# Performance work log

Measured on AMD Instinct MI355X. Metric: run time of the kernel, lower is better.

Reference implementation:

```python
import jax, jax.numpy as jnp
import numpy as np

E, H, T_MAX = 1024, 16, 2048
HS = E // H
EPS = 1e-5


def _layernorm(x, g, b):
    m = jnp.mean(x, axis=-1, keepdims=True)
    v = jnp.mean(jnp.square(x - m), axis=-1, keepdims=True)
    return (x - m) * jax.lax.rsqrt(v + EPS) * g + b


def setup_inputs() -> dict:
    key = jax.random.key(0)
    ks = jax.random.split(key, 8)
    B, T = 2, 2048
    s = 0.02
    return {
        "x": jax.random.normal(ks[0], (B, T, E), jnp.float32),
        "ln1_g": jnp.ones((E,), jnp.float32),
        "ln1_b": jnp.zeros((E,), jnp.float32),
        "Wk": jax.random.normal(ks[1], (H, E, HS), jnp.float32) * s,  # stacked per-head key weights (x @ Wk)
        "Wv": jax.random.normal(ks[2], (H, E, HS), jnp.float32) * s,
        "Wproj": jax.random.normal(ks[3], (E, E), jnp.float32) * s,
        "bproj": jnp.zeros((E,), jnp.float32),
        "ln2_g": jnp.ones((E,), jnp.float32),
        "ln2_b": jnp.zeros((E,), jnp.float32),
        "W1": jax.random.normal(ks[4], (E, 4 * E), jnp.float32) * s,
        "b1": jnp.zeros((4 * E,), jnp.float32),
        "W2": jax.random.normal(ks[5], (4 * E, E), jnp.float32) * s,
        "b2": jnp.zeros((E,), jnp.float32),
    }


def reference(x, ln1_g, ln1_b, Wk, Wv, Wproj, bproj, ln2_g, ln2_b, W1, b1, W2, b2):
    B, T, C = x.shape
    h = _layernorm(x, ln1_g, ln1_b)
    # NOTE: original code uses the KEY projection for both q and k (q = self.key(x))
    k = jnp.einsum('bte,hed->bhtd', h, Wk)
    q = k
    wei = jnp.einsum('bhtd,bhsd->bhts', q, k) * (C ** -0.5)  # scale by full n_embd, as in source
    causal = jnp.tril(jnp.ones((T, T), bool))
    wei = jnp.where(causal, wei, -jnp.inf)
    # source applies softmax over dim=1 (the query/row axis of the TxT matrix)
    wei = jax.nn.softmax(wei, axis=2)
    v = jnp.einsum('bte,hed->bhtd', h, Wv)
    attn = jnp.einsum('bhts,bhsd->bhtd', wei, v)          # [B,H,T,HS]
    attn = attn.transpose(0, 2, 1, 3).reshape(B, T, C)    # concat heads
    x = x + attn @ Wproj + bproj
    h2 = _layernorm(x, ln2_g, ln2_b)
    x = x + jax.nn.relu(h2 @ W1 + b1) @ W2 + b2
    return x
```

## Files before the change

kernel.cpp:

```cpp
#include <hip/hip_runtime.h>

using bf16x8 = __attribute__((ext_vector_type(8))) __bf16;
using f32x4  = __attribute__((ext_vector_type(4))) float;

__device__ __forceinline__ f32x4 mfma16(bf16x8 a, bf16x8 b, f32x4 c) {
  return __builtin_amdgcn_mfma_f32_16x16x32_bf16(a, b, c, 0, 0, 0);
}

__device__ __forceinline__ unsigned short f2bf(float f) {
  union { float f; unsigned int u; } x; x.f = f;
  unsigned int u = x.u + 0x7FFFu + ((x.u >> 16) & 1u);
  return (unsigned short)(u >> 16);
}

__device__ __forceinline__ unsigned int cvtpk_bf16(float lo, float hi) {
  unsigned int r;
  asm("v_cvt_pk_bf16_f32 %0, %1, %2" : "=v"(r) : "v"(lo), "v"(hi));
  return r;
}

__device__ __forceinline__ float fexp2(float x) {
#if __has_builtin(__builtin_amdgcn_exp2f)
  return __builtin_amdgcn_exp2f(x);
#else
  float r; asm("v_exp_f32 %0, %1" : "=v"(r) : "v"(x)); return r;
#endif
}

__device__ __forceinline__ void gl_lds16(const unsigned short* g, unsigned short* l) {
  __builtin_amdgcn_global_load_lds(
      (__attribute__((address_space(1))) void*)(g),
      (__attribute__((address_space(3))) void*)(l), 16, 0, 0);
}

__device__ __forceinline__ bf16x8 rdsw64(const unsigned short* base, int r, int ch) {
  int c = ch ^ (r & 7);
  return *reinterpret_cast<const bf16x8*>(base + ((size_t)r * 8 + c) * 8);
}

__global__ __launch_bounds__(256) void transpose_cvt(const float* __restrict__ in,
                                                     unsigned short* __restrict__ out,
                                                     int R, int C) {
  __shared__ float t[32][33];
  int b = blockIdx.z;
  const float* inb = in + (size_t)b * R * C;
  unsigned short* outb = out + (size_t)b * R * C;
  int tx = threadIdx.x & 31, ty = threadIdx.x >> 5;
  int c0 = blockIdx.x * 32, r0 = blockIdx.y * 32;
#pragma unroll
  for (int i = 0; i < 4; ++i)
    t[ty + i * 8][tx] = inb[(size_t)(r0 + ty + i * 8) * C + c0 + tx];
  __syncthreads();
#pragma unroll
  for (int i = 0; i < 4; ++i)
    outb[(size_t)(c0 + ty + i * 8) * R + r0 + tx] = f2bf(t[tx][ty + i * 8]);
}

__global__ __launch_bounds__(256) void ln_bf16(const float* __restrict__ x,
                                               const float* __restrict__ g,
                                               const float* __restrict__ bta,
                                               unsigned short* __restrict__ out) {
  int row = blockIdx.x, tid = threadIdx.x;
  float4 v = reinterpret_cast<const float4*>(x + (size_t)row * 1024)[tid];
  float s = v.x + v.y + v.z + v.w;
  float s2 = v.x * v.x + v.y * v.y + v.z * v.z + v.w * v.w;
#pragma unroll
  for (int m = 1; m < 64; m <<= 1) { s += __shfl_xor(s, m); s2 += __shfl_xor(s2, m); }
  __shared__ float red[8];
  int w = tid >> 6;
  if ((tid & 63) == 0) { red[w] = s; red[w + 4] = s2; }
  __syncthreads();
  s  = red[0] + red[1] + red[2] + red[3];
  s2 = red[4] + red[5] + red[6] + red[7];
  float mean = s * (1.f / 1024.f);
  float var  = s2 * (1.f / 1024.f) - mean * mean;
  float rstd = rsqrtf(var + 1e-5f);
  float4 gv = reinterpret_cast<const float4*>(g)[tid];
  float4 bv = reinterpret_cast<const float4*>(bta)[tid];
  ushort4 o;
  o.x = f2bf((v.x - mean) * rstd * gv.x + bv.x);
  o.y = f2bf((v.y - mean) * rstd * gv.y + bv.y);
  o.z = f2bf((v.z - mean) * rstd * gv.z + bv.z);
  o.w = f2bf((v.w - mean) * rstd * gv.w + bv.w);
  reinterpret_cast<ushort4*>(out + (size_t)row * 1024)[tid] = o;
}

__device__ __forceinline__ void stage_half(const unsigned short* gbase, int K,
                                           unsigned short* lds, int tid) {
#pragma unroll
  for (int j = 0; j < 2; ++j) {
    int lr = j * 64 + (tid >> 3);
    int c  = (tid & 7) ^ (lr & 7);
    gl_lds16(gbase + (size_t)lr * K + c * 8, lds + (size_t)(j * 512 + tid) * 8);
  }
}

__device__ __forceinline__ bf16x8 rdfrag(const unsigned short* base, int r, int k) {
  return *reinterpret_cast<const bf16x8*>(base + ((size_t)r * 8 + (k ^ (r & 7))) * 8);
}

__global__ __launch_bounds__(512, 2) void gemm256_relu(const unsigned short* __restrict__ A,
                                                       const unsigned short* __restrict__ Bt,
                                                       unsigned short* __restrict__ C,
                                                       const float* __restrict__ bias,
                                                       int M, int N, int K) {
  __shared__ __align__(16) unsigned short LA[2][256 * 64];
  __shared__ __align__(16) unsigned short LB[2][256 * 64];
  int tid = threadIdx.x, lane = tid & 63, w = tid >> 6;
  int l15 = lane & 15, lh = lane >> 4;
  int wr = (w >> 2) * 128, wc = (w & 3) * 64;
  int bid = blockIdx.x;
  int xcd = bid & 7, g = bid >> 3;
  int bm = (xcd >> 1) * 4 + (g >> 3);
  int bn = (xcd & 1) * 8 + (g & 7);
  const unsigned short* Ab = A + (size_t)(bm * 256) * K;
  const unsigned short* Bb = Bt + (size_t)(bn * 256) * K;
  f32x4 acc[8][4] = {};
  int NT = K >> 6;
  stage_half(Ab, K, &LA[0][0], tid);
  stage_half(Ab + (size_t)128 * K, K, &LA[0][128 * 64], tid);
  stage_half(Bb, K, &LB[0][0], tid);
  stage_half(Bb + (size_t)128 * K, K, &LB[0][128 * 64], tid);
  asm volatile("s_waitcnt vmcnt(0)" ::: "memory");
  __builtin_amdgcn_s_barrier();
  for (int t = 0; t < NT; ++t) {
    int cur = t & 1;
    const unsigned short* la = &LA[cur][0];
    const unsigned short* lb = &LB[cur][0];
    unsigned short* na = &LA[cur ^ 1][0];
    unsigned short* nb = &LB[cur ^ 1][0];
    int k0n = (t + 1) << 6;
    bool more = (t + 1 < NT);
    bf16x8 bfr[4][2];
#pragma unroll
    for (int q = 0; q < 4; ++q) {
      if (more) {
        if (q == 0)      stage_half(Ab + k0n, K, na, tid);
        else if (q == 1) stage_half(Ab + (size_t)128 * K + k0n, K, na + 128 * 64, tid);
        else if (q == 2) stage_half(Bb + k0n, K, nb, tid);
        else             stage_half(Bb + (size_t)128 * K + k0n, K, nb + 128 * 64, tid);
      }
      if (q == 0) {
        if (more) asm volatile("s_waitcnt vmcnt(2)" ::: "memory");
        else      asm volatile("s_waitcnt vmcnt(0)" ::: "memory");
        __builtin_amdgcn_s_barrier();
      }
      bf16x8 aq[2][2];
#pragma unroll
      for (int i = 0; i < 2; ++i)
#pragma unroll
        for (int kk = 0; kk < 2; ++kk)
          aq[i][kk] = rdfrag(la, wr + q * 32 + i * 16 + l15, kk * 4 + lh);
      if (q == 0) {
#pragma unroll
        for (int ni = 0; ni < 4; ++ni)
#pragma unroll
          for (int kk = 0; kk < 2; ++kk)
            bfr[ni][kk] = rdfrag(lb, wc + ni * 16 + l15, kk * 4 + lh);
      }
      if (q != 0) __builtin_amdgcn_s_barrier();
      __builtin_amdgcn_s_setprio(1);
#pragma unroll
      for (int kk = 0; kk < 2; ++kk)
#pragma unroll
        for (int i = 0; i < 2; ++i)
#pragma unroll
          for (int ni = 0; ni < 4; ++ni)
            acc[q * 2 + i][ni] = mfma16(aq[i][kk], bfr[ni][kk], acc[q * 2 + i][ni]);
      __builtin_amdgcn_s_setprio(0);
      __builtin_amdgcn_s_barrier();
    }
  }
#pragma unroll
  for (int mi = 0; mi < 8; ++mi)
#pragma unroll
    for (int ni = 0; ni < 4; ++ni) {
      int row0 = bm * 256 + wr + mi * 16 + lh * 4;
      int col  = bn * 256 + wc + ni * 16 + l15;
      float bv = bias[col];
#pragma unroll
      for (int r = 0; r < 4; ++r) {
        float v = fmaxf(acc[mi][ni][r] + bv, 0.f);
        C[(size_t)(row0 + r) * N + col] = f2bf(v);
      }
    }
}

#define GBK 128
#define KSCL 0.04508422f

__device__ __forceinline__ bf16x8 rd128(const unsigned short* base, int r, int ch) {
  int c = ch ^ ((r & 7) << 1);
  return *reinterpret_cast<const bf16x8*>(base + (size_t)r * GBK + c * 8);
}

template<int TM, int MODE>
__global__ __launch_bounds__(256) void gemm_bf16(const unsigned short* __restrict__ A,
                                                 const unsigned short* __restrict__ Bt,
                                                 void* __restrict__ Cout,
                                                 unsigned short* __restrict__ Cout2,
                                                 const float* __restrict__ bias,
                                                 const float* __restrict__ resid,
                                                 const float* __restrict__ scvec,
                                                 int M, int N, int K) {
  constexpr int MI = TM / 32;
  constexpr int AJ = TM / 16;
  __shared__ __align__(16) unsigned short Sh[(TM + 128) * GBK];
  unsigned short* As = Sh;
  unsigned short* Bs = Sh + TM * GBK;
  int tid = threadIdx.x;
  int lane = tid & 63, w = tid >> 6;
  int l15 = lane & 15, lh = lane >> 4;
  int wr = (w >> 1) * (TM / 2), wc = (w & 1) * 64;
  int nblk = N >> 7;
  int rows = M / TM;
  int bm, bn;
  if (nblk == 8 && (rows & 7) == 0) {
    int bid = blockIdx.x;
    int xcd = bid & 7, g = bid >> 3;
    bm = xcd * (rows >> 3) + (g >> 3);
    bn = g & 7;
  } else {
    bm = blockIdx.x / nblk; bn = blockIdx.x % nblk;
  }
  const unsigned short* ApJ[AJ];
  const unsigned short* BpJ[8];
#pragma unroll
  for (int j = 0; j < AJ; ++j) {
    int row = j * 16 + (tid >> 4);
    int ch  = (tid & 15) ^ ((row & 7) << 1);
    ApJ[j] = A + (size_t)(bm * TM + row) * K + ch * 8;
  }
#pragma unroll
  for (int j = 0; j < 8; ++j) {
    int row = j * 16 + (tid >> 4);
    int ch  = (tid & 15) ^ ((row & 7) << 1);
    BpJ[j] = Bt + (size_t)(bn * 128 + row) * K + ch * 8;
  }
  f32x4 acc[MI][4] = {};
  for (int k0 = 0; k0 < K; k0 += GBK) {
#pragma unroll
    for (int j = 0; j < AJ; ++j)
      gl_lds16(ApJ[j] + k0, &As[(j * 256 + tid) * 8]);
#pragma unroll
    for (int j = 0; j < 8; ++j)
      gl_lds16(BpJ[j] + k0, &Bs[(j * 256 + tid) * 8]);
    __syncthreads();
    bf16x8 af[MI][4], bfr[4][4];
#pragma unroll
    for (int i = 0; i < MI; ++i)
#pragma unroll
      for (int kk = 0; kk < 4; ++kk)
        af[i][kk] = rd128(As, wr + i * 16 + l15, kk * 4 + lh);
#pragma unroll
    for (int i = 0; i < 4; ++i)
#pragma unroll
      for (int kk = 0; kk < 4; ++kk)
        bfr[i][kk] = rd128(Bs, wc + i * 16 + l15, kk * 4 + lh);
#pragma unroll
    for (int kk = 0; kk < 4; ++kk)
#pragma unroll
      for (int mi = 0; mi < MI; ++mi)
#pragma unroll
        for (int ni = 0; ni < 4; ++ni)
          acc[mi][ni] = mfma16(af[mi][kk], bfr[ni][kk], acc[mi][ni]);
    __syncthreads();
  }
  if constexpr (MODE == 3) {
#pragma unroll
    for (int mi = 0; mi < MI; ++mi) {
#pragma unroll
      for (int ni = 0; ni < 4; ++ni) {
        int tl = wr + mi * 16 + lh * 4;
        int dl = wc + ni * 16 + l15;
        int colg = bn * 128 + dl;
        int bb = bm >> 5, hh = colg >> 6;
        const float* sp = scvec + (size_t)(bb * 16 + hh) * 2048 + (bm & 31) * 64 + tl;
        float4 rs = *reinterpret_cast<const float4*>(sp);
        unsigned int p0 = f2bf(acc[mi][ni][0] * rs.x) | ((unsigned int)f2bf(acc[mi][ni][1] * rs.y) << 16);
        unsigned int p1 = f2bf(acc[mi][ni][2] * rs.z) | ((unsigned int)f2bf(acc[mi][ni][3] * rs.w) << 16);
        uint2 pk = {p0, p1};
        *reinterpret_cast<uint2*>(&Sh[dl * 64 + (tl ^ ((dl & 7) << 3))]) = pk;
      }
    }
    __syncthreads();
    int dr = tid >> 1, th = (tid & 1) * 32;
    int bb = bm >> 5, tbase = (bm & 31) * 64;
    size_t colg = bn * 128 + dr;
    unsigned short* Vt = (unsigned short*)Cout;
#pragma unroll
    for (int j = 0; j < 4; ++j) {
      int t = th + j * 8;
      int4 v = *reinterpret_cast<const int4*>(&Sh[dr * 64 + (t ^ ((dr & 7) << 3))]);
      *reinterpret_cast<int4*>(&Vt[((size_t)bb * 1024 + colg) * 2048 + tbase + t]) = v;
    }
  } else {
#pragma unroll
    for (int mi = 0; mi < MI; ++mi) {
#pragma unroll
      for (int ni = 0; ni < 4; ++ni) {
        int row0 = bm * TM + wr + mi * 16 + lh * 4;
        int col  = bn * 128 + wc + ni * 16 + l15;
        float bv = (MODE == 2) ? 0.f : bias[col];
#pragma unroll
        for (int r = 0; r < 4; ++r) {
          int row = row0 + r;
          float v = acc[mi][ni][r] + bv;
          if constexpr (MODE == 0) {
            v += resid[(size_t)row * N + col];
            ((float*)Cout)[(size_t)row * N + col] = v;
          } else {
            ((unsigned short*)Cout)[(size_t)row * N + col] = f2bf(v);
            Cout2[(size_t)row * N + col] = f2bf(v * KSCL);
          }
        }
      }
    }
  }
}

__global__ __launch_bounds__(512) void attn_stats(const unsigned short* __restrict__ Kb,
                                                  const unsigned short* __restrict__ Kbs,
                                                  float* __restrict__ colrcp) {
  __shared__ __align__(16) unsigned short Kt[2][64 * 64];
  int bid = blockIdx.x;
  int q = bid >> 8, x = (bid >> 5) & 7, bh = bid & 31;
  int b = bh >> 4, h = bh & 15;
  int sb = q ? (15 - x) : x;
  int tid = threadIdx.x, lane = tid & 63, w = tid >> 6;
  int l15 = lane & 15, lh = lane >> 4;
  int s0 = sb * 128, sw = s0 + w * 16;
  const unsigned short* Kp  = Kb  + ((size_t)b * 2048) * 1024 + h * 64;
  const unsigned short* Kps = Kbs + ((size_t)b * 2048) * 1024 + h * 64;
  bf16x8 as[2];
#pragma unroll
  for (int kc = 0; kc < 2; ++kc)
    as[kc] = *reinterpret_cast<const bf16x8*>(Kp + (size_t)(sw + l15) * 1024 + kc * 32 + (lh << 3));
  int srow = tid >> 3;
  int sch  = (tid & 7) ^ (srow & 7);
  const unsigned short* ksrc = Kps + (size_t)srow * 1024 + sch * 8;
  gl_lds16(ksrc + (size_t)s0 * 1024, &Kt[0][tid * 8]);
  __syncthreads();
  float l[4] = {0.f, 0.f, 0.f, 0.f};
  int nt = 32 - 2 * sb;
  for (int it = 0; it < nt; ++it) {
    int t0 = s0 + it * 64;
    int cur = it & 1;
    if (it + 1 < nt)
      gl_lds16(ksrc + (size_t)(t0 + 64) * 1024, &Kt[cur ^ 1][tid * 8]);
    if (t0 + 63 >= sw) {
      bool dmask = (t0 < sw + 16);
#pragma unroll
      for (int tf = 0; tf < 4; ++tf) {
        int tr = tf * 16 + l15;
        bf16x8 bt0 = rdsw64(&Kt[cur][0], tr, lh);
        bf16x8 bt1 = rdsw64(&Kt[cur][0], tr, 4 + lh);
        f32x4 z = {};
        f32x4 sa = mfma16(as[1], bt1, mfma16(as[0], bt0, z));
        int tg = t0 + tr;
#pragma unroll
        for (int r = 0; r < 4; ++r) {
          float e = fexp2(sa[r]);
          if (dmask) { int sg = sw + lh * 4 + r; e = (tg >= sg) ? e : 0.f; }
          l[r] += e;
        }
      }
    }
    __syncthreads();
  }
#pragma unroll
  for (int m = 1; m < 16; m <<= 1)
#pragma unroll
    for (int r = 0; r < 4; ++r)
      l[r] += __shfl_xor(l[r], m);
  if (l15 == 0) {
#pragma unroll
    for (int r = 0; r < 4; ++r)
      colrcp[(size_t)bh * 2048 + sw + lh * 4 + r] = 1.f / l[r];
  }
}

__global__ __launch_bounds__(512) void attn_pv(const unsigned short* __restrict__ Kb,
                                               const unsigned short* __restrict__ Kbs,
                                               const unsigned short* __restrict__ Vt,
                                               unsigned short* __restrict__ attn) {
  __shared__ __align__(16) unsigned short Ks[2][64 * 64];
  __shared__ __align__(16) unsigned short Vs[2][64 * 64];
  __shared__ __align__(16) unsigned short Pl[8][16][68];
  int bid = blockIdx.x;
  int q = bid >> 8, x = (bid >> 5) & 7, bh = bid & 31;
  int b = bh >> 4, h = bh & 15;
  int tb = q ? (15 - x) : x;
  int tid = threadIdx.x, lane = tid & 63, w = tid >> 6;
  int l15 = lane & 15, lh = lane >> 4;
  int t0 = tb * 128, tw = t0 + w * 16;
  const unsigned short* Kp  = Kb  + ((size_t)b * 2048) * 1024 + h * 64;
  const unsigned short* Kps = Kbs + ((size_t)b * 2048) * 1024 + h * 64;
  const unsigned short* Vp  = Vt + (size_t)bh * 64 * 2048;
  bf16x8 at[2];
#pragma unroll
  for (int kc = 0; kc < 2; ++kc)
    at[kc] = *reinterpret_cast<const bf16x8*>(Kp + (size_t)(tw + l15) * 1024 + kc * 32 + (lh << 3));
  int srow = tid >> 3;
  int sch  = (tid & 7) ^ (srow & 7);
  const unsigned short* ksrc = Kps + (size_t)srow * 1024 + sch * 8;
  const unsigned short* vsrc = Vp + (size_t)srow * 2048 + sch * 8;
  gl_lds16(ksrc, &Ks[0][tid * 8]);
  gl_lds16(vsrc, &Vs[0][tid * 8]);
  __syncthreads();
  f32x4 acc[4] = {};
  int nt = 2 * tb + 2;
  for (int it = 0; it < nt; ++it) {
    int s0 = it * 64;
    int cur = it & 1;
    if (it + 1 < nt) {
      gl_lds16(ksrc + (size_t)(s0 + 64) * 1024, &Ks[cur ^ 1][tid * 8]);
      gl_lds16(vsrc + (s0 + 64), &Vs[cur ^ 1][tid * 8]);
    }
    if (s0 <= tw + 15) {
      bool dmask = (s0 + 63 > tw);
#pragma unroll
      for (int sf = 0; sf < 4; ++sf) {
        int sr = sf * 16 + l15;
        bf16x8 ks0 = rdsw64(&Ks[cur][0], sr, lh);
        bf16x8 ks1 = rdsw64(&Ks[cur][0], sr, 4 + lh);
        f32x4 z = {};
        f32x4 sa = mfma16(ks1, at[1], mfma16(ks0, at[0], z));
        float pe[4];
#pragma unroll
        for (int r = 0; r < 4; ++r) {
          float p = fexp2(sa[r]);
          if (dmask) {
            int sg = s0 + sf * 16 + lh * 4 + r;
            int tg = tw + l15;
            p = (sg <= tg) ? p : 0.f;
          }
          pe[r] = p;
        }
        unsigned int u0 = cvtpk_bf16(pe[0], pe[1]);
        unsigned int u1 = cvtpk_bf16(pe[2], pe[3]);
        unsigned long long pk = (unsigned long long)u0 | ((unsigned long long)u1 << 32);
        *reinterpret_cast<unsigned long long*>(&Pl[w][l15][sf * 16 + lh * 4]) = pk;
      }
#pragma unroll
      for (int c2 = 0; c2 < 2; ++c2) {
        bf16x8 pa = *reinterpret_cast<const bf16x8*>(&Pl[w][l15][c2 * 32 + (lh << 3)]);
#pragma unroll
        for (int nf = 0; nf < 4; ++nf) {
          int dr = nf * 16 + l15;
          bf16x8 vb = rdsw64(&Vs[cur][0], dr, c2 * 4 + lh);
          acc[nf] = mfma16(pa, vb, acc[nf]);
        }
      }
    }
    __syncthreads();
  }
#pragma unroll
  for (int nf = 0; nf < 4; ++nf)
#pragma unroll
    for (int r = 0; r < 4; ++r) {
      int t = tw + lh * 4 + r;
      attn[(size_t)(b * 2048 + t) * 1024 + h * 64 + nf * 16 + l15] = f2bf(acc[nf][r]);
    }
}

extern "C" void kernel_launch(void* const* d_in, const int* in_sizes, int n_in,
                              void* d_out, int out_size, void* d_ws, size_t ws_size,
                              hipStream_t stream) {
  (void)in_sizes; (void)n_in; (void)out_size; (void)ws_size;
  const float* x     = (const float*)d_in[0];
  const float* ln1_g = (const float*)d_in[1];
  const float* ln1_b = (const float*)d_in[2];
  const float* Wk    = (const float*)d_in[3];
  const float* Wv    = (const float*)d_in[4];
  const float* Wproj = (const float*)d_in[5];
  const float* bproj = (const float*)d_in[6];
  const float* ln2_g = (const float*)d_in[7];
  const float* ln2_b = (const float*)d_in[8];
  const float* W1    = (const float*)d_in[9];
  const float* b1    = (const float*)d_in[10];
  const float* W2    = (const float*)d_in[11];
  const float* b2    = (const float*)d_in[12];
  float* out = (float*)d_out;

  char* ws = (char*)d_ws;
  size_t off = 0;
  auto alloc = [&](size_t bytes) { void* p = ws + off; off += (bytes + 255) & ~(size_t)255; return p; };
  unsigned short* bufA = (unsigned short*)alloc((size_t)4096 * 1024 * 2);
  unsigned short* wk_t = (unsigned short*)alloc((size_t)1024 * 1024 * 2);
  unsigned short* wv_t = (unsigned short*)alloc((size_t)1024 * 1024 * 2);
  unsigned short* wp_t = (unsigned short*)alloc((size_t)1024 * 1024 * 2);
  unsigned short* w1_t = (unsigned short*)alloc((size_t)1024 * 4096 * 2);
  unsigned short* w2_t = (unsigned short*)alloc((size_t)4096 * 1024 * 2);
  unsigned short* Kb   = (unsigned short*)alloc((size_t)4096 * 1024 * 2);
  unsigned short* Kbs  = (unsigned short*)alloc((size_t)4096 * 1024 * 2);
  unsigned short* Vt   = (unsigned short*)alloc((size_t)4096 * 1024 * 2);
  float* colrcp = (float*)alloc((size_t)32 * 2048 * 4);
  float* y      = (float*)alloc((size_t)4096 * 1024 * 4);
  unsigned short* act = (unsigned short*)alloc((size_t)4096 * 4096 * 2);

  dim3 b256(256), b512(512);
  transpose_cvt<<<dim3(2, 32, 16), b256, 0, stream>>>(Wk, wk_t, 1024, 64);
  transpose_cvt<<<dim3(2, 32, 16), b256, 0, stream>>>(Wv, wv_t, 1024, 64);
  transpose_cvt<<<dim3(32, 32, 1), b256, 0, stream>>>(Wproj, wp_t, 1024, 1024);
  transpose_cvt<<<dim3(128, 32, 1), b256, 0, stream>>>(W1, w1_t, 1024, 4096);
  transpose_cvt<<<dim3(32, 128, 1), b256, 0, stream>>>(W2, w2_t, 4096, 1024);

  ln_bf16<<<4096, b256, 0, stream>>>(x, ln1_g, ln1_b, bufA);
  gemm_bf16<64, 2><<<512, b256, 0, stream>>>(bufA, wk_t, Kb, Kbs, nullptr, nullptr, nullptr, 4096, 1024, 1024);
  attn_stats<<<512, b512, 0, stream>>>(Kb, Kbs, colrcp);
  gemm_bf16<64, 3><<<512, b256, 0, stream>>>(bufA, wv_t, Vt, nullptr, nullptr, nullptr, colrcp, 4096, 1024, 1024);
  attn_pv<<<512, b512, 0, stream>>>(Kb, Kbs, Vt, bufA);
  gemm_bf16<64, 0><<<512, b256, 0, stream>>>(bufA, wp_t, y, nullptr, bproj, x, nullptr, 4096, 1024, 1024);
  ln_bf16<<<4096, b256, 0, stream>>>(y, ln2_g, ln2_b, bufA);
  gemm256_relu<<<256, dim3(512), 0, stream>>>(bufA, w1_t, act, b1, 4096, 4096, 1024);
  gemm_bf16<64, 0><<<512, b256, 0, stream>>>(act, w2_t, out, nullptr, b2, y, nullptr, 4096, 1024, 4096);
}
```

Before: 238.3 us.

## Software-pipeline P·V one tile behind QK exp in attention kernel

Restructures the attention P·V kernel so each iteration computes the exp(QK) tile for block it while doing the P·V MFMAs for block it-1. V gets a triple buffer and P a double buffer per wave, so the two stages can overlap without extra barriers. The tile-order mapping is also flipped so the heavier causal blocks are scheduled first. Costs more LDS, which may lower occupancy, and adds an epilogue.

```diff
diff --git a/kernel.cpp b/kernel.cpp
--- a/kernel.cpp
+++ b/kernel.cpp
@@ -385,12 +385,12 @@
                                                const unsigned short* __restrict__ Vt,
                                                unsigned short* __restrict__ attn) {
   __shared__ __align__(16) unsigned short Ks[2][64 * 64];
-  __shared__ __align__(16) unsigned short Vs[2][64 * 64];
-  __shared__ __align__(16) unsigned short Pl[8][16][68];
+  __shared__ __align__(16) unsigned short Vs[3][64 * 64];
+  __shared__ __align__(16) unsigned short Pl[8][2][16][68];
   int bid = blockIdx.x;
   int q = bid >> 8, x = (bid >> 5) & 7, bh = bid & 31;
   int b = bh >> 4, h = bh & 15;
-  int tb = q ? (15 - x) : x;
+  int tb = q ? x : (15 - x);
   int tid = threadIdx.x, lane = tid & 63, w = tid >> 6;
   int l15 = lane & 15, lh = lane >> 4;
   int t0 = tb * 128, tw = t0 + w * 16;
@@ -405,25 +405,25 @@
   int sch  = (tid & 7) ^ (srow & 7);
   const unsigned short* ksrc = Kps + (size_t)srow * 1024 + sch * 8;
   const unsigned short* vsrc = Vp + (size_t)srow * 2048 + sch * 8;
+  int nt = 2 * tb + 2;
   gl_lds16(ksrc, &Ks[0][tid * 8]);
   gl_lds16(vsrc, &Vs[0][tid * 8]);
   __syncthreads();
   f32x4 acc[4] = {};
-  int nt = 2 * tb + 2;
   for (int it = 0; it < nt; ++it) {
     int s0 = it * 64;
-    int cur = it & 1;
+    const unsigned short* ksCur = &Ks[it & 1][0];
     if (it + 1 < nt) {
-      gl_lds16(ksrc + (size_t)(s0 + 64) * 1024, &Ks[cur ^ 1][tid * 8]);
-      gl_lds16(vsrc + (s0 + 64), &Vs[cur ^ 1][tid * 8]);
+      gl_lds16(ksrc + (size_t)(s0 + 64) * 1024, &Ks[(it + 1) & 1][tid * 8]);
+      gl_lds16(vsrc + (s0 + 64), &Vs[(it + 1) % 3][tid * 8]);
     }
     if (s0 <= tw + 15) {
       bool dmask = (s0 + 63 > tw);
 #pragma unroll
       for (int sf = 0; sf < 4; ++sf) {
         int sr = sf * 16 + l15;
-        bf16x8 ks0 = rdsw64(&Ks[cur][0], sr, lh);
-        bf16x8 ks1 = rdsw64(&Ks[cur][0], sr, 4 + lh);
+        bf16x8 ks0 = rdsw64(ksCur, sr, lh);
+        bf16x8 ks1 = rdsw64(ksCur, sr, 4 + lh);
         f32x4 z = {};
         f32x4 sa = mfma16(ks1, at[1], mfma16(ks0, at[0], z));
         float pe[4];
@@ -440,20 +440,42 @@
         unsigned int u0 = cvtpk_bf16(pe[0], pe[1]);
         unsigned int u1 = cvtpk_bf16(pe[2], pe[3]);
         unsigned long long pk = (unsigned long long)u0 | ((unsigned long long)u1 << 32);
-        *reinterpret_cast<unsigned long long*>(&Pl[w][l15][sf * 16 + lh * 4]) = pk;
-      }
+        *reinterpret_cast<unsigned long long*>(&Pl[w][it & 1][l15][sf * 16 + lh * 4]) = pk;
+      }
+    }
+    if (it > 0) {
+      int pit = it - 1;
+      if (pit * 64 <= tw + 15) {
+        const unsigned short* vsPrev = &Vs[pit % 3][0];
+#pragma unroll
+        for (int c2 = 0; c2 < 2; ++c2) {
+          bf16x8 pa = *reinterpret_cast<const bf16x8*>(&Pl[w][pit & 1][l15][c2 * 32 + (lh << 3)]);
+#pragma unroll
+          for (int nf = 0; nf < 4; ++nf) {
+            int dr = nf * 16 + l15;
+            bf16x8 vb = rdsw64(vsPrev, dr, c2 * 4 + lh);
+            acc[nf] = mfma16(pa, vb, acc[nf]);
+          }
+        }
+      }
+    }
+    __syncthreads();
+  }
+  {
+    int pit = nt - 1;
+    if (pit * 64 <= tw + 15) {
+      const unsigned short* vsPrev = &Vs[pit % 3][0];
 #pragma unroll
       for (int c2 = 0; c2 < 2; ++c2) {
-        bf16x8 pa = *reinterpret_cast<const bf16x8*>(&Pl[w][l15][c2 * 32 + (lh << 3)]);
+        bf16x8 pa = *reinterpret_cast<const bf16x8*>(&Pl[w][pit & 1][l15][c2 * 32 + (lh << 3)]);
 #pragma unroll
         for (int nf = 0; nf < 4; ++nf) {
           int dr = nf * 16 + l15;
-          bf16x8 vb = rdsw64(&Vs[cur][0], dr, c2 * 4 + lh);
+          bf16x8 vb = rdsw64(vsPrev, dr, c2 * 4 + lh);
           acc[nf] = mfma16(pa, vb, acc[nf]);
         }
       }
     }
-    __syncthreads();
   }
 #pragma unroll
   for (int nf = 0; nf < 4; ++nf)
```

New measurement: 240.1 us. About the same (+0.8%).
